# Performance work log

Measured on AMD Instinct MI355X. Metric: run time of the kernel, lower is better.

## Reference

```python
import jax, jax.numpy as jnp
import numpy as np

TEMP = 0.07
IGNORE = 255
NUM_CLS = 150   # ADE Challenge classes
VOCAB = 512     # size of the dense idx_star -> cls_idx LUT
B, D, H, W = 4, 512, 256, 256


def setup_inputs() -> dict:
    key = jax.random.key(0)
    k1, k2, k3 = jax.random.split(key, 3)
    pred_embs = jax.random.normal(k1, (B, D, H, W), dtype=jnp.float32)
    # class text embeddings, L2-normalized per class (as in load_ade_challenge_info)
    cls = jax.random.normal(k2, (NUM_CLS, D), dtype=jnp.float32)
    cls_embs = cls / jnp.linalg.norm(cls, axis=1, keepdims=True)
    # idx_star semantic label map, shape (B, 1, H, W)
    idx_star_map = jax.random.randint(k3, (B, 1, H, W), 0, VOCAB, dtype=jnp.int32)
    # dense LUT replacing the python dict idx_star2cls_idx:
    # first NUM_CLS idx_star values map to class indices, the rest are ignored (255)
    ar = jnp.arange(VOCAB, dtype=jnp.int32)
    lut = jnp.where(ar < NUM_CLS, ar, IGNORE).astype(jnp.int32)
    return {"pred_embs": pred_embs, "cls_embs": cls_embs,
            "idx_star_map": idx_star_map, "lut": lut}


def reference(pred_embs, cls_embs, idx_star_map, lut):
    # --- label remap: single gather replaces the per-unique-value mask loop ---
    labels = lut[idx_star_map[:, 0]]                       # (B, H, W) int32
    # --- 1x1 conv == per-pixel dot product with class embeddings ---
    sim = jnp.einsum('bdhw,kd->bkhw', pred_embs, cls_embs) / TEMP  # (B, K, H, W)
    # --- cross-entropy with ignore_index=255 (mean over valid pixels) ---
    logp = jax.nn.log_softmax(sim, axis=1)                 # (B, K, H, W)
    valid = labels != IGNORE
    safe = jnp.where(valid, labels, 0)
    nll = -jnp.take_along_axis(logp, safe[:, None], axis=1)[:, 0]  # (B, H, W)
    n_valid = jnp.sum(valid).astype(nll.dtype)
    return jnp.sum(jnp.where(valid, nll, 0.0)) / n_valid
```

## Files before the change

### kernel.cpp

```cpp
#include <hip/hip_runtime.h>
#include <hip/hip_bf16.h>


#define NUM_CLS 150
#define NT_TILES 10
#define D_DIM   512
#define HW_DIM  65536
#define IGNORE_L 255

typedef __attribute__((ext_vector_type(8))) short bf16x8;
typedef __attribute__((ext_vector_type(4))) float f32x4;
typedef __attribute__((ext_vector_type(4))) unsigned int u32x4;

#define GLOAD16(gsrc, ldst) \
    __builtin_amdgcn_global_load_lds((const __attribute__((address_space(1))) void*)(gsrc), \
                                     (__attribute__((address_space(3))) void*)(ldst), 16, 0, 0)

static __device__ __forceinline__ short f2bf(float f) {
    __hip_bfloat16 h = __float2bfloat16(f);
    return __builtin_bit_cast(short, h);
}

__global__ void rsl_pack_cls(const float* __restrict__ cls,
                             unsigned short* __restrict__ packed,
                             double* __restrict__ ws_sum,
                             unsigned long long* __restrict__ ws_cnt)
{
    int t = blockIdx.x * 256 + threadIdx.x;
    if (t == 0) { ws_sum[0] = 0.0; ws_cnt[0] = 0ull; }
    if (t >= 16 * NT_TILES * 64) return;
    int s  = t / (NT_TILES * 64);
    int r  = t - s * (NT_TILES * 64);
    int nt = r >> 6;
    int l  = r & 63;
    int c  = nt * 16 + (l & 15);
    int k  = s * 32 + (l >> 4) * 8;
    unsigned short v[8];
#pragma unroll
    for (int j = 0; j < 8; ++j)
        v[j] = (c < NUM_CLS) ? (unsigned short)f2bf(cls[c * D_DIM + k + j]) : (unsigned short)0;
    u32x4 w;
#pragma unroll
    for (int q = 0; q < 4; ++q)
        w[q] = (unsigned int)v[2 * q] | ((unsigned int)v[2 * q + 1] << 16);
    *(u32x4*)(packed + (size_t)(s * NT_TILES + nt) * 512 + (size_t)l * 8) = w;
}

__global__ __launch_bounds__(256, 2)
void rsl_mfma(const float* __restrict__ pred,
              const unsigned short* __restrict__ packed,
              const int*   __restrict__ idx,
              const int*   __restrict__ lut,
              double* __restrict__ ws_sum,
              unsigned long long* __restrict__ ws_cnt)
{
    __shared__ float sP[3][32][128];

    const int lane = threadIdx.x & 63;
    const int wid  = threadIdx.x >> 6;
    const int row  = lane & 15;
    const int g    = lane >> 4;

    const int pixbase = blockIdx.x * 128;
    const int b  = pixbase >> 16;
    const int p0 = pixbase & 0xFFFF;
    const float* predb = pred + (size_t)b * D_DIM * HW_DIM;
    const int pxl = (lane & 31) * 4;
    const int dl  = lane >> 5;

    f32x4 acc[2][NT_TILES] = {};
    bf16x8 cfA[NT_TILES], cfB[NT_TILES];

#define STAGE(ss, q) do { \
    _Pragma("unroll") \
    for (int tt = 0; tt < 4; ++tt) { \
        const int t_ = wid * 4 + tt; \
        GLOAD16(predb + (size_t)((ss) * 32 + 2 * t_ + dl) * HW_DIM \
                      + (p0 + (pxl ^ ((t_ >> 2) << 3))), \
                &sP[q][2 * t_][0]); \
    } } while (0)

#define LOADCLS(ss, cf) do { \
    const unsigned short* cb_ = packed + (size_t)((ss) * NT_TILES) * 512 + (size_t)lane * 8; \
    _Pragma("unroll") \
    for (int nt = 0; nt < NT_TILES; ++nt) cf[nt] = *(const bf16x8*)(cb_ + nt * 512); \
    } while (0)

    LOADCLS(0, cfA);
    asm volatile("" ::: "memory");
    STAGE(0, 0);
    asm volatile("" ::: "memory");
    STAGE(1, 1);

#define ITER(s, CUR, NXT) do { \
    if ((s) < 15) asm volatile("s_waitcnt vmcnt(4)" ::: "memory"); \
    else          asm volatile("s_waitcnt vmcnt(0)" ::: "memory"); \
    __builtin_amdgcn_sched_barrier(0); \
    __builtin_amdgcn_s_barrier(); \
    __builtin_amdgcn_sched_barrier(0); \
    if ((s) + 1 < 16) { LOADCLS((s) + 1, NXT); } \
    asm volatile("" ::: "memory"); \
    if ((s) + 2 < 16) { STAGE((s) + 2, ((s) + 2) % 3); } \
    bf16x8 pf[2]; \
    _Pragma("unroll") \
    for (int mt = 0; mt < 2; ++mt) \
        _Pragma("unroll") \
        for (int j = 0; j < 8; ++j) \
            pf[mt][j] = f2bf(sP[(s) % 3][g * 8 + j][(wid * 32 + mt * 16 + row) ^ (g << 3)]); \
    _Pragma("unroll") \
    for (int nt = 0; nt < NT_TILES; ++nt) { \
        _Pragma("unroll") \
        for (int mt = 0; mt < 2; ++mt) \
            acc[mt][nt] = __builtin_amdgcn_mfma_f32_16x16x32_bf16(pf[mt], CUR[nt], acc[mt][nt], 0, 0, 0); \
    } } while (0)

#pragma unroll
    for (int h = 0; h < 8; ++h) {
        ITER(2 * h,     cfA, cfB);
        ITER(2 * h + 1, cfB, cfA);
    }

    const float invT = 1.0f / 0.07f;
    float local_sum = 0.f;
    int   local_cnt = 0;
#pragma unroll
    for (int mt = 0; mt < 2; ++mt) {
#pragma unroll
        for (int j = 0; j < 4; ++j) {
            const int pixg = pixbase + wid * 32 + mt * 16 + g * 4 + j;
            const int lab  = lut[idx[pixg]];
            const bool valid = (lab != IGNORE_L);

            float m = -1e30f;
#pragma unroll
            for (int nt = 0; nt < NT_TILES; ++nt) {
                int c = nt * 16 + row;
                float v = (c < NUM_CLS) ? acc[mt][nt][j] : -1e30f;
                m = fmaxf(m, v);
            }
#pragma unroll
            for (int o = 8; o >= 1; o >>= 1) m = fmaxf(m, __shfl_xor(m, o));

            float ssum = 0.f, slab = 0.f;
#pragma unroll
            for (int nt = 0; nt < NT_TILES; ++nt) {
                int c = nt * 16 + row;
                if (c < NUM_CLS) {
                    float v = acc[mt][nt][j];
                    ssum += __expf((v - m) * invT);
                    slab += (c == lab) ? v : 0.f;
                }
            }
#pragma unroll
            for (int o = 8; o >= 1; o >>= 1) {
                ssum += __shfl_xor(ssum, o);
                slab += __shfl_xor(slab, o);
            }
            if (row == 0 && valid) {
                local_sum += (m - slab) * invT + __logf(ssum);
                local_cnt += 1;
            }
        }
    }

#pragma unroll
    for (int o = 32; o >= 1; o >>= 1) {
        local_sum += __shfl_down(local_sum, o);
        local_cnt += __shfl_down(local_cnt, o);
    }
    __shared__ float sv[4];
    __shared__ int   sc[4];
    if (lane == 0) { sv[wid] = local_sum; sc[wid] = local_cnt; }
    __syncthreads();
    if (threadIdx.x == 0) {
        float tv = sv[0] + sv[1] + sv[2] + sv[3];
        int   tc = sc[0] + sc[1] + sc[2] + sc[3];
        atomicAdd(ws_sum, (double)tv);
        atomicAdd(ws_cnt, (unsigned long long)tc);
    }
}

__global__ void rsl_final(const double* __restrict__ ws_sum,
                          const unsigned long long* __restrict__ ws_cnt,
                          float* __restrict__ out)
{
    if (threadIdx.x == 0) {
        double c = (double)ws_cnt[0];
        out[0] = (float)(ws_sum[0] / (c > 0.0 ? c : 1.0));
    }
}

extern "C" void kernel_launch(void* const* d_in, const int* in_sizes, int n_in,
                              void* d_out, int out_size, void* d_ws, size_t ws_size,
                              hipStream_t stream)
{
    const float* pred = (const float*)d_in[0];
    const float* cls  = (const float*)d_in[1];
    const int*   idx  = (const int*)d_in[2];
    const int*   lut  = (const int*)d_in[3];
    float* out = (float*)d_out;

    double* wsd = (double*)d_ws;
    unsigned long long* wsc = (unsigned long long*)((char*)d_ws + 8);
    unsigned short* packed = (unsigned short*)((char*)d_ws + 1024);

    rsl_pack_cls<<<40, 256, 0, stream>>>(cls, packed, wsd, wsc);

    const int total = 4 * HW_DIM;
    rsl_mfma<<<total / 128, 256, 0, stream>>>(pred, packed, idx, lut, wsd, wsc);
    rsl_final<<<1, 64, 0, stream>>>(wsd, wsc, out);
}
```

Measured before the change: 144.4 us.

## Stage class-embedding fragments through LDS instead of per-lane register prefetch

```diff
diff --git a/kernel.cpp b/kernel.cpp
--- a/kernel.cpp
+++ b/kernel.cpp
@@ -54,7 +54,8 @@
               double* __restrict__ ws_sum,
               unsigned long long* __restrict__ ws_cnt)
 {
-    __shared__ float sP[3][32][128];
+    __shared__ float          sP[3][32][128];
+    __shared__ unsigned short sC[2][NT_TILES][512];
 
     const int lane = threadIdx.x & 63;
     const int wid  = threadIdx.x >> 6;
@@ -69,56 +70,64 @@
     const int dl  = lane >> 5;
 
     f32x4 acc[2][NT_TILES] = {};
-    bf16x8 cfA[NT_TILES], cfB[NT_TILES];
-
-#define STAGE(ss, q) do { \
+
+#define STAGEP(ss) do { \
+    const float* srcb_ = predb + (size_t)((ss) * 32) * HW_DIM; \
     _Pragma("unroll") \
     for (int tt = 0; tt < 4; ++tt) { \
         const int t_ = wid * 4 + tt; \
-        GLOAD16(predb + (size_t)((ss) * 32 + 2 * t_ + dl) * HW_DIM \
-                      + (p0 + (pxl ^ ((t_ >> 2) << 3))), \
-                &sP[q][2 * t_][0]); \
+        GLOAD16(srcb_ + (size_t)(2 * t_ + dl) * HW_DIM + (p0 + (pxl ^ ((t_ >> 2) << 3))), \
+                &sP[(ss) % 3][2 * t_][0]); \
     } } while (0)
 
-#define LOADCLS(ss, cf) do { \
-    const unsigned short* cb_ = packed + (size_t)((ss) * NT_TILES) * 512 + (size_t)lane * 8; \
-    _Pragma("unroll") \
-    for (int nt = 0; nt < NT_TILES; ++nt) cf[nt] = *(const bf16x8*)(cb_ + nt * 512); \
+#define STAGEC(ss) do { \
+    for (int nt = wid; nt < NT_TILES; nt += 4) \
+        GLOAD16(packed + (size_t)((ss) * NT_TILES + nt) * 512 + (size_t)lane * 8, \
+                &sC[(ss) & 1][nt][0]); \
     } while (0)
 
-    LOADCLS(0, cfA);
-    asm volatile("" ::: "memory");
-    STAGE(0, 0);
-    asm volatile("" ::: "memory");
-    STAGE(1, 1);
-
-#define ITER(s, CUR, NXT) do { \
-    if ((s) < 15) asm volatile("s_waitcnt vmcnt(4)" ::: "memory"); \
-    else          asm volatile("s_waitcnt vmcnt(0)" ::: "memory"); \
-    __builtin_amdgcn_sched_barrier(0); \
-    __builtin_amdgcn_s_barrier(); \
-    __builtin_amdgcn_sched_barrier(0); \
-    if ((s) + 1 < 16) { LOADCLS((s) + 1, NXT); } \
-    asm volatile("" ::: "memory"); \
-    if ((s) + 2 < 16) { STAGE((s) + 2, ((s) + 2) % 3); } \
+#define COMPUTE(s) do { \
+    const int pb_ = (s) % 3; const int cb_ = (s) & 1; \
     bf16x8 pf[2]; \
     _Pragma("unroll") \
     for (int mt = 0; mt < 2; ++mt) \
         _Pragma("unroll") \
         for (int j = 0; j < 8; ++j) \
-            pf[mt][j] = f2bf(sP[(s) % 3][g * 8 + j][(wid * 32 + mt * 16 + row) ^ (g << 3)]); \
+            pf[mt][j] = f2bf(sP[pb_][g * 8 + j][(wid * 32 + mt * 16 + row) ^ (g << 3)]); \
     _Pragma("unroll") \
     for (int nt = 0; nt < NT_TILES; ++nt) { \
+        bf16x8 cf = *(const bf16x8*)&sC[cb_][nt][lane * 8]; \
         _Pragma("unroll") \
         for (int mt = 0; mt < 2; ++mt) \
-            acc[mt][nt] = __builtin_amdgcn_mfma_f32_16x16x32_bf16(pf[mt], CUR[nt], acc[mt][nt], 0, 0, 0); \
+            acc[mt][nt] = __builtin_amdgcn_mfma_f32_16x16x32_bf16(pf[mt], cf, acc[mt][nt], 0, 0, 0); \
     } } while (0)
 
-#pragma unroll
-    for (int h = 0; h < 8; ++h) {
-        ITER(2 * h,     cfA, cfB);
-        ITER(2 * h + 1, cfB, cfA);
-    }
+    STAGEC(0);
+    asm volatile("" ::: "memory");
+    STAGEP(0);
+    asm volatile("" ::: "memory");
+    STAGEP(1);
+
+    for (int s = 0; s < 14; ++s) {
+        asm volatile("s_waitcnt vmcnt(4)" ::: "memory");
+        __builtin_amdgcn_s_barrier();
+        asm volatile("" ::: "memory");
+        STAGEC(s + 1);
+        asm volatile("" ::: "memory");
+        STAGEP(s + 2);
+        asm volatile("" ::: "memory");
+        COMPUTE(s);
+    }
+    asm volatile("s_waitcnt vmcnt(4)" ::: "memory");
+    __builtin_amdgcn_s_barrier();
+    asm volatile("" ::: "memory");
+    STAGEC(15);
+    asm volatile("" ::: "memory");
+    COMPUTE(14);
+    asm volatile("s_waitcnt vmcnt(0)" ::: "memory");
+    __builtin_amdgcn_s_barrier();
+    asm volatile("" ::: "memory");
+    COMPUTE(15);
 
     const float invT = 1.0f / 0.07f;
     float local_sum = 0.f;
```

New measurement: 139.2 us. -3.6%, faster.
